# Kernel optimization log

Hardware: AMD Instinct MI355X
Metric: run time of the kernel (lower is better)

Reference implementation:

```python
import jax, jax.numpy as jnp
import numpy as np

N_NODES = 50000
N_EDGES = 600000
N_REL = 3
VALUE_NUM, TEXT_NUM, FEAT, CLASSES = 16, 768, 128, 2
N_IDX = 10000


def setup_inputs() -> dict:
    key = jax.random.key(0)
    ks = jax.random.split(key, 24)
    s = 0.05
    inp = {
        'value_feature': jax.random.normal(ks[0], (N_NODES, VALUE_NUM), jnp.float32),
        'text_feature': jax.random.normal(ks[1], (N_NODES, TEXT_NUM), jnp.float32),
        'fc1_w': jax.random.normal(ks[2], (VALUE_NUM, FEAT), jnp.float32) * s,
        'fc1_b': jnp.zeros((FEAT,), jnp.float32),
        'fc2_w': jax.random.normal(ks[3], (TEXT_NUM, FEAT), jnp.float32) * s,
        'fc2_b': jnp.zeros((FEAT,), jnp.float32),
        'relu_w': jax.random.normal(ks[4], (2 * FEAT, FEAT), jnp.float32) * s,
        'relu_b': jnp.zeros((FEAT,), jnp.float32),
        'rgcn1_wrel': jax.random.normal(ks[5], (N_REL, FEAT, FEAT), jnp.float32) * s,
        'rgcn1_wroot': jax.random.normal(ks[6], (FEAT, FEAT), jnp.float32) * s,
        'rgcn1_b': jnp.zeros((FEAT,), jnp.float32),
        'rgcn2_wrel': jax.random.normal(ks[7], (N_REL, FEAT, FEAT), jnp.float32) * s,
        'rgcn2_wroot': jax.random.normal(ks[8], (FEAT, FEAT), jnp.float32) * s,
        'rgcn2_b': jnp.zeros((FEAT,), jnp.float32),
        'fc3_w': jax.random.normal(ks[9], (FEAT, CLASSES), jnp.float32) * s,
        'fc3_b': jnp.zeros((CLASSES,), jnp.float32),
        'edge_index': jax.random.randint(ks[10], (2, N_EDGES), 0, N_NODES, jnp.int64 if jax.config.jax_enable_x64 else jnp.int32),
        'edge_type': jax.random.randint(ks[11], (N_EDGES,), 0, N_REL, jnp.int32),
        'idx': jax.random.randint(ks[12], (N_IDX,), 0, N_NODES, jnp.int32),
    }
    return inp


def _rgcn(x, w_rel, w_root, b, src, dst, etype, n_nodes):
    # Per-relation transform: [R, N, D]
    xw = jnp.einsum('nd,rde->rne', x, w_rel)
    msg = xw[etype, src]  # gather per-edge messages [E, D]
    # mean aggregation per (relation, dst) pair (PyG RGCNConv default aggr='mean')
    deg = jnp.zeros((N_REL, n_nodes), x.dtype).at[etype, dst].add(1.0)
    norm = 1.0 / jnp.maximum(deg[etype, dst], 1.0)  # [E]
    agg = jnp.zeros((n_nodes, x.shape[1]), x.dtype).at[dst].add(msg * norm[:, None])
    return agg + x @ w_root + b


def reference(value_feature, text_feature, fc1_w, fc1_b, fc2_w, fc2_b,
              relu_w, relu_b, rgcn1_wrel, rgcn1_wroot, rgcn1_b,
              rgcn2_wrel, rgcn2_wroot, rgcn2_b, fc3_w, fc3_b,
              edge_index, edge_type, idx):
    src, dst = edge_index[0], edge_index[1]
    v = value_feature @ fc1_w + fc1_b
    t = text_feature @ fc2_w + fc2_b
    h = jnp.concatenate([v, t], axis=1)
    h = jax.nn.leaky_relu(h @ relu_w + relu_b, negative_slope=0.01)
    # dropout is identity at eval
    h = _rgcn(h, rgcn1_wrel, rgcn1_wroot, rgcn1_b, src, dst, edge_type, h.shape[0])
    h = _rgcn(h, rgcn2_wrel, rgcn2_wroot, rgcn2_b, src, dst, edge_type, h.shape[0])
    return h[idx] @ fc3_w + fc3_b
```

## Files before the change

kernel.cpp:

```cpp
#include <hip/hip_runtime.h>
#include <hip/hip_bf16.h>

typedef __attribute__((ext_vector_type(8))) short s16x8;
typedef __attribute__((ext_vector_type(4))) float f32x4;
typedef unsigned short u16;
typedef unsigned int u32;

constexpr int NN = 50000;
constexpr int NE = 600000;
constexpr int NIDX = 10000;

__device__ inline u16 f2b(float x) {
    __hip_bfloat16 h = __float2bfloat16(x);
    return *(u16*)&h;
}

__device__ inline s16x8 pack8(float4 a, float4 b) {
    s16x8 r;
    r[0] = (short)f2b(a.x); r[1] = (short)f2b(a.y);
    r[2] = (short)f2b(a.z); r[3] = (short)f2b(a.w);
    r[4] = (short)f2b(b.x); r[5] = (short)f2b(b.y);
    r[6] = (short)f2b(b.z); r[7] = (short)f2b(b.w);
    return r;
}

__device__ inline void gl_lds16(const void* gptr, void* lptr) {
    __builtin_amdgcn_global_load_lds(
        (const __attribute__((address_space(1))) char*)gptr,
        (__attribute__((address_space(3))) char*)lptr, 16, 0, 0);
}

template <int N> __device__ inline void vmwait() {
    asm volatile("s_waitcnt vmcnt(%0)" :: "n"(N) : "memory");
}
__device__ inline void barrier_nodrains() {
    __builtin_amdgcn_sched_barrier(0);
    __builtin_amdgcn_s_barrier();
    __builtin_amdgcn_sched_barrier(0);
}


__global__ void k_setup(const float* __restrict__ vf,
                        const float* __restrict__ fc1w, const float* __restrict__ fc2w,
                        const float* __restrict__ reluw,
                        const float* __restrict__ fc1b, const float* __restrict__ fc2b,
                        const float* __restrict__ relub,
                        const float* __restrict__ w1rel, const float* __restrict__ w1root,
                        const float* __restrict__ w2rel, const float* __restrict__ w2root,
                        float* __restrict__ vfp, u16* __restrict__ WTin,
                        float* __restrict__ bcomb, u16* __restrict__ WT1, u16* __restrict__ WT2,
                        int* __restrict__ zero_region, int* __restrict__ mark) {
    int b = blockIdx.x, t = threadIdx.x;
    if (b < 6250) {
        int i = b * 256 + t;
        int n = i >> 5, c = i & 31;
        vfp[i] = c < 16 ? vf[n * 16 + c] : 0.f;
    } else if (b < 7050) {
        if (t < 128) {
            int k = b - 6250, c = t;
            float s = 0.f;
            if (k < 768) {
                for (int j = 0; j < 128; ++j) s += fc2w[k * 128 + j] * reluw[(128 + j) * 128 + c];
            } else if (k < 784) {
                int kk = k - 768;
                for (int j = 0; j < 128; ++j) s += fc1w[kk * 128 + j] * reluw[j * 128 + c];
            }
            WTin[c * 800 + k] = f2b(s);
        }
    } else if (b == 7050) {
        if (t < 128) {
            int c = t;
            float s = relub[c];
            for (int j = 0; j < 128; ++j) {
                s += fc1b[j] * reluw[j * 128 + c];
                s += fc2b[j] * reluw[(128 + j) * 128 + c];
            }
            bcomb[c] = s;
        }
    } else if (b < 7563) {
        if (t < 128) {
            int s = b - 7051, c = t;
            float v = (s < 384) ? w1rel[(size_t)s * 128 + c] : w1root[(size_t)(s - 384) * 128 + c];
            WT1[c * 512 + s] = f2b(v);
        }
    } else if (b < 8075) {
        if (t < 128) {
            int s = b - 7563, c = t;
            float v = (s < 384) ? w2rel[(size_t)s * 128 + c] : w2root[(size_t)(s - 384) * 128 + c];
            WT2[c * 512 + s] = f2b(v);
        }
    } else if (b < 9052) {
        int i = (b - 8075) * 256 + t;
        if (i < 250002) zero_region[i] = 0;
    } else {
        int i = (b - 9052) * 256 + t;
        if (i < NN) mark[i] = 0;
    }
}


__global__ void k_hist_mark(const int* __restrict__ ei, const int* __restrict__ et,
                            int* __restrict__ deg_node, int* __restrict__ deg_rel,
                            const int* __restrict__ idx, int* __restrict__ mark,
                            int* __restrict__ cnt2, int* __restrict__ list) {
    int b = blockIdx.x;
    if (b < 2344) {
        int e = b * 256 + threadIdx.x;
        if (e < NE) {
            int dst = ei[NE + e];
            int r = et[e];
            atomicAdd(&deg_node[dst], 1);
            atomicAdd(&deg_rel[r * NN + dst], 1);
        }
    } else {
        int i = (b - 2344) * 256 + threadIdx.x;
        if (i < NIDX) {
            int n = idx[i];
            if (atomicExch(&mark[n], 1) == 0) {
                int p = atomicAdd(cnt2, 1);
                list[p] = n;
            }
        }
    }
}


__global__ void k_alloc_norm(const int* __restrict__ deg_node, int* __restrict__ baseoff,
                             int* __restrict__ counter, const int* __restrict__ deg_rel,
                             float* __restrict__ normf) {
    int b = blockIdx.x;
    if (b < 196) {
        int i = b * 256 + threadIdx.x;
        int lane = threadIdx.x & 63;
        int d = (i < NN) ? deg_node[i] : 0;
        int scan = d;
        for (int off = 1; off < 64; off <<= 1) {
            int t = __shfl_up(scan, off, 64);
            if (lane >= off) scan += t;
        }
        int total = __shfl(scan, 63, 64);
        int wbase = 0;
        if (lane == 63) wbase = atomicAdd(counter, total);
        wbase = __shfl(wbase, 63, 64);
        if (i < NN) baseoff[i] = wbase + scan - d;
    } else {
        int i = (b - 196) * 256 + threadIdx.x;
        if (i < 3 * NN) normf[i] = 1.0f / (float)max(deg_rel[i], 1);
    }
}

__global__ void k_fill(const int* __restrict__ ei, const int* __restrict__ et,
                       const int* __restrict__ baseoff, int* __restrict__ cursor,
                       int* __restrict__ elist) {
    int e = blockIdx.x * 256 + threadIdx.x;
    if (e >= NE) return;
    int dst = ei[NE + e];
    int src = ei[e];
    int r = et[e];
    int pos = atomicAdd(&cursor[dst], 1);
    elist[baseoff[dst] + pos] = src | (r << 20);
}


__global__ __launch_bounds__(64) void k_agg(const u16* __restrict__ x, u16* __restrict__ A,
                                            const int* __restrict__ elist,
                                            const int* __restrict__ baseoff,
                                            const int* __restrict__ deg_node,
                                            const float* __restrict__ normf) {
    int n = blockIdx.x;
    int lane = threadIdx.x;
    float a0x = 0.f, a0y = 0.f, a1x = 0.f, a1y = 0.f, a2x = 0.f, a2y = 0.f;
    int nb = deg_node[n];
    int b0 = baseoff[n];
    for (int i = 0; i < nb; ++i) {
        int p = elist[b0 + i];
        int src = p & 0xFFFFF;
        int r = p >> 20;
        u32 pair = *(const u32*)&x[(size_t)src * 128 + lane * 2];
        float vx = __uint_as_float((pair & 0xFFFFu) << 16);
        float vy = __uint_as_float((pair >> 16) << 16);
        if (r == 0)      { a0x += vx; a0y += vy; }
        else if (r == 1) { a1x += vx; a1y += vy; }
        else             { a2x += vx; a2y += vy; }
    }
    float n0 = normf[n], n1 = normf[NN + n], n2 = normf[2 * NN + n];
    u32* Ao = (u32*)&A[(size_t)n * 384];
    Ao[lane]        = (u32)f2b(a0x * n0) | ((u32)f2b(a0y * n0) << 16);
    Ao[64 + lane]   = (u32)f2b(a1x * n1) | ((u32)f2b(a1y * n1) << 16);
    Ao[128 + lane]  = (u32)f2b(a2x * n2) | ((u32)f2b(a2y * n2) << 16);
}

__global__ __launch_bounds__(64) void k_agg2(const u16* __restrict__ x, u16* __restrict__ A2buf,
                                             const int* __restrict__ elist,
                                             const int* __restrict__ baseoff,
                                             const int* __restrict__ deg_node,
                                             const float* __restrict__ normf,
                                             const int* __restrict__ list,
                                             const int* __restrict__ cnt2) {
    int i = blockIdx.x;
    if (i >= *cnt2) return;
    int n = list[i];
    int lane = threadIdx.x;
    float a0x = 0.f, a0y = 0.f, a1x = 0.f, a1y = 0.f, a2x = 0.f, a2y = 0.f;
    int nb = deg_node[n];
    int b0 = baseoff[n];
    for (int e = 0; e < nb; ++e) {
        int p = elist[b0 + e];
        int src = p & 0xFFFFF;
        int r = p >> 20;
        u32 pair = *(const u32*)&x[(size_t)src * 128 + lane * 2];
        float vx = __uint_as_float((pair & 0xFFFFu) << 16);
        float vy = __uint_as_float((pair >> 16) << 16);
        if (r == 0)      { a0x += vx; a0y += vy; }
        else if (r == 1) { a1x += vx; a1y += vy; }
        else             { a2x += vx; a2y += vy; }
    }
    float n0 = normf[n], n1 = normf[NN + n], n2 = normf[2 * NN + n];
    u32* Ao = (u32*)&A2buf[(size_t)i * 384];
    Ao[lane]        = (u32)f2b(a0x * n0) | ((u32)f2b(a0y * n0) << 16);
    Ao[64 + lane]   = (u32)f2b(a1x * n1) | ((u32)f2b(a1y * n1) << 16);
    Ao[128 + lane]  = (u32)f2b(a2x * n2) | ((u32)f2b(a2y * n2) << 16);
}


template <typename TA, int K1T, int K2T, bool LRELU, bool LIST>
__device__ __forceinline__ void gemm_body(const TA* __restrict__ A1, int lda1,
                                          const TA* __restrict__ A2, int lda2,
                                          const u16* __restrict__ WT, int ldwt,
                                          const float* __restrict__ bias,
                                          u16* __restrict__ out, int Nin,
                                          const int* __restrict__ list,
                                          const int* __restrict__ cntp) {
    constexpr int KT = K1T + K2T;
    constexpr int ABYTES = 64 * 32 * (int)sizeof(TA);
    constexpr int TILEB = ABYTES + 8192;
    constexpr int OPW = (sizeof(TA) == 4) ? 4 : 3;
    __shared__ alignas(128) char lds[3][TILEB];

    const int N = LIST ? *cntp : Nin;
    const int m0 = blockIdx.x * 64;
    if (LIST && m0 >= N) return;

    const int tid = threadIdx.x;
    const int w = tid >> 6, lane = tid & 63;
    const int wr = w >> 1, wc = w & 1;
    const int lq = lane >> 4, lr = lane & 15;

    auto stage = [&](int j) {
        char* base = lds[j % 3];
        int kt = j;
        if constexpr (sizeof(TA) == 4) {
#pragma unroll
            for (int jj = 0; jj < 2; ++jj) {
                int row = w * 16 + jj * 8 + (lane >> 3);
                int s = lane & 7;
                int chunk = s ^ (row & 7);
                int rg = min(m0 + row, N - 1);
                const float* g;
                if (kt < K1T) g = (const float*)A1 + (size_t)rg * lda1 + kt * 32 + chunk * 4;
                else          g = (const float*)A2 + (size_t)rg * lda2 + (kt - K1T) * 32 + chunk * 4;
                gl_lds16(g, base + w * 2048 + jj * 1024);
            }
        } else {
            int row = w * 16 + (lane >> 2);
            int s = lane & 3;
            int chunk = s ^ ((row >> 1) & 3);
            int rg = min(m0 + row, N - 1);
            const u16* g;
            if (kt < K1T) {
                g = (const u16*)A1 + (size_t)rg * lda1 + kt * 32 + chunk * 8;
            } else {
                int node = LIST ? list[rg] : rg;
                g = (const u16*)A2 + (size_t)node * lda2 + (kt - K1T) * 32 + chunk * 8;
            }
            gl_lds16(g, base + w * 1024);
        }
#pragma unroll
        for (int jj = 0; jj < 2; ++jj) {
            int col = w * 32 + jj * 16 + (lane >> 2);
            int s = lane & 3;
            int chunk = s ^ ((col >> 1) & 3);
            const u16* g = WT + (size_t)col * ldwt + kt * 32 + chunk * 8;
            gl_lds16(g, base + ABYTES + w * 2048 + jj * 1024);
        }
    };

    f32x4 acc[2][4] = {};

    auto compute = [&](int j) {
        char* base = lds[j % 3];
        s16x8 af[2];
#pragma unroll
        for (int i = 0; i < 2; ++i) {
            int row = wr * 32 + i * 16 + lr;
            if constexpr (sizeof(TA) == 4) {
                int m = row & 7;
                float4 f0 = *(const float4*)(base + row * 128 + (((2 * lq) ^ m) * 16));
                float4 f1 = *(const float4*)(base + row * 128 + (((2 * lq + 1) ^ m) * 16));
                af[i] = pack8(f0, f1);
            } else {
                int sl = lq ^ ((row >> 1) & 3);
                af[i] = *(const s16x8*)(base + row * 64 + sl * 16);
            }
        }
#pragma unroll
        for (int j4 = 0; j4 < 4; ++j4) {
            int col = wc * 64 + j4 * 16 + lr;
            int sl = lq ^ ((col >> 1) & 3);
            s16x8 bf = *(const s16x8*)(base + ABYTES + col * 64 + sl * 16);
#pragma unroll
            for (int i = 0; i < 2; ++i)
                acc[i][j4] = __builtin_amdgcn_mfma_f32_16x16x32_bf16(af[i], bf, acc[i][j4], 0, 0, 0);
        }
    };

    stage(0); stage(1);
#pragma unroll 1
    for (int j = 0; j < KT - 1; ++j) {
        vmwait<OPW>();
        barrier_nodrains();
        if (j + 2 < KT) stage(j + 2);
        compute(j);
    }
    vmwait<0>();
    barrier_nodrains();
    compute(KT - 1);

#pragma unroll
    for (int i = 0; i < 2; ++i) {
#pragma unroll
        for (int q = 0; q < 4; ++q) {
            int grow = m0 + wr * 32 + i * 16 + lq * 4 + q;
            if (grow < N) {
                int orow = LIST ? list[grow] : grow;
#pragma unroll
                for (int j = 0; j < 4; ++j) {
                    int col = wc * 64 + j * 16 + lr;
                    float v = acc[i][j][q] + bias[col];
                    if (LRELU) v = v > 0.f ? v : 0.01f * v;
                    out[(size_t)orow * 128 + col] = f2b(v);
                }
            }
        }
    }
}

__global__ __launch_bounds__(256) void k_gemm_in(const float* __restrict__ A1, int lda1,
                                                 const float* __restrict__ A2, int lda2,
                                                 const u16* __restrict__ WT, int ldwt,
                                                 const float* __restrict__ bias,
                                                 u16* __restrict__ out, int N) {
    gemm_body<float, 24, 1, true, false>(A1, lda1, A2, lda2, WT, ldwt, bias, out, N, nullptr, nullptr);
}
__global__ __launch_bounds__(256) void k_gemm_r1(const u16* __restrict__ A1, int lda1,
                                                 const u16* __restrict__ A2, int lda2,
                                                 const u16* __restrict__ WT, int ldwt,
                                                 const float* __restrict__ bias,
                                                 u16* __restrict__ out, int N) {
    gemm_body<u16, 12, 4, false, false>(A1, lda1, A2, lda2, WT, ldwt, bias, out, N, nullptr, nullptr);
}
__global__ __launch_bounds__(256) void k_gemm_r2(const u16* __restrict__ A1, int lda1,
                                                 const u16* __restrict__ A2, int lda2,
                                                 const u16* __restrict__ WT, int ldwt,
                                                 const float* __restrict__ bias,
                                                 u16* __restrict__ out,
                                                 const int* __restrict__ list,
                                                 const int* __restrict__ cnt2) {
    gemm_body<u16, 12, 4, false, true>(A1, lda1, A2, lda2, WT, ldwt, bias, out, NIDX, list, cnt2);
}


__global__ __launch_bounds__(256) void k_out(const u16* __restrict__ h, const int* __restrict__ idx,
                                             const float* __restrict__ fc3w,
                                             const float* __restrict__ fc3b,
                                             float* __restrict__ out, int M) {
    int w = threadIdx.x >> 6;
    int lane = threadIdx.x & 63;
    int row = blockIdx.x * 4 + w;
    if (row >= M) return;
    int n = idx[row];
    u32 pair = *(const u32*)&h[(size_t)n * 128 + lane * 2];
    float v0 = __uint_as_float((pair & 0xFFFFu) << 16);
    float v1 = __uint_as_float((pair >> 16) << 16);
    float4 wv = *(const float4*)&fc3w[lane * 4];
    float s0 = v0 * wv.x + v1 * wv.z;
    float s1 = v0 * wv.y + v1 * wv.w;
    for (int off = 32; off >= 1; off >>= 1) {
        s0 += __shfl_xor(s0, off, 64);
        s1 += __shfl_xor(s1, off, 64);
    }
    if (lane == 0) {
        out[row * 2] = s0 + fc3b[0];
        out[row * 2 + 1] = s1 + fc3b[1];
    }
}


extern "C" void kernel_launch(void* const* d_in, const int* in_sizes, int n_in,
                              void* d_out, int out_size, void* d_ws, size_t ws_size,
                              hipStream_t stream) {
    const float* vf    = (const float*)d_in[0];
    const float* tf    = (const float*)d_in[1];
    const float* fc1w  = (const float*)d_in[2];
    const float* fc1b  = (const float*)d_in[3];
    const float* fc2w  = (const float*)d_in[4];
    const float* fc2b  = (const float*)d_in[5];
    const float* reluw = (const float*)d_in[6];
    const float* relub = (const float*)d_in[7];
    const float* w1rel = (const float*)d_in[8];
    const float* w1root= (const float*)d_in[9];
    const float* b1    = (const float*)d_in[10];
    const float* w2rel = (const float*)d_in[11];
    const float* w2root= (const float*)d_in[12];
    const float* b2    = (const float*)d_in[13];
    const float* fc3w  = (const float*)d_in[14];
    const float* fc3b  = (const float*)d_in[15];
    const int* ei      = (const int*)d_in[16];
    const int* et      = (const int*)d_in[17];
    const int* idx     = (const int*)d_in[18];
    float* out = (float*)d_out;

    char* W = (char*)d_ws;
    const size_t OFF_WTIN  = 0;
    const size_t OFF_WT1   = 204800;
    const size_t OFF_WT2   = 335872;
    const size_t OFF_BCOMB = 466944;
    const size_t OFF_DEGN  = 467456;
    const size_t OFF_CUR   = 667456;
    const size_t OFF_DEGR  = 867456;
    const size_t OFF_CNT   = 1467456;
    const size_t OFF_CNT2  = 1467460;
    const size_t OFF_BASE  = 1467712;
    const size_t OFF_NORM  = 1667712;
    const size_t OFF_ELIST = 2267712;
    const size_t OFF_A     = 4667712;
    const size_t OFF_H0    = 43067712;
    const size_t OFF_H1    = 55867712;
    const size_t OFF_H2    = 68667712;
    const size_t OFF_VFPAD = 81467712;
    const size_t OFF_LIST  = 87867712;
    const size_t OFF_A2    = 87907712;
    const size_t OFF_MARK  = 95587712;

    u16* WTin   = (u16*)(W + OFF_WTIN);
    u16* WT1    = (u16*)(W + OFF_WT1);
    u16* WT2    = (u16*)(W + OFF_WT2);
    float* bcomb= (float*)(W + OFF_BCOMB);
    int* degn   = (int*)(W + OFF_DEGN);
    int* cur    = (int*)(W + OFF_CUR);
    int* degr   = (int*)(W + OFF_DEGR);
    int* cnt    = (int*)(W + OFF_CNT);
    int* cnt2   = (int*)(W + OFF_CNT2);
    int* base   = (int*)(W + OFF_BASE);
    float* normf= (float*)(W + OFF_NORM);
    int* elist  = (int*)(W + OFF_ELIST);
    u16* Abuf   = (u16*)(W + OFF_A);
    u16* h0     = (u16*)(W + OFF_H0);
    u16* h1     = (u16*)(W + OFF_H1);
    u16* h2     = (u16*)(W + OFF_H2);
    float* vfp  = (float*)(W + OFF_VFPAD);
    int* list   = (int*)(W + OFF_LIST);
    u16* A2buf  = (u16*)(W + OFF_A2);
    int* mark   = (int*)(W + OFF_MARK);

    const int GRID_GEMM = (NN + 63) / 64;
    const int GRID_G2   = (NIDX + 63) / 64;

    k_setup<<<9248, 256, 0, stream>>>(vf, fc1w, fc2w, reluw, fc1b, fc2b, relub,
                                      w1rel, w1root, w2rel, w2root,
                                      vfp, WTin, bcomb, WT1, WT2, degn, mark);

    k_gemm_in<<<GRID_GEMM, 256, 0, stream>>>(tf, 768, vfp, 32, WTin, 800, bcomb, h0, NN);

    k_hist_mark<<<2384, 256, 0, stream>>>(ei, et, degn, degr, idx, mark, cnt2, list);
    k_alloc_norm<<<782, 256, 0, stream>>>(degn, base, cnt, degr, normf);
    k_fill<<<(NE + 255) / 256, 256, 0, stream>>>(ei, et, base, cur, elist);

    k_agg<<<NN, 64, 0, stream>>>(h0, Abuf, elist, base, degn, normf);
    k_gemm_r1<<<GRID_GEMM, 256, 0, stream>>>(Abuf, 384, h0, 128, WT1, 512, b1, h1, NN);

    k_agg2<<<NIDX, 64, 0, stream>>>(h1, A2buf, elist, base, degn, normf, list, cnt2);
    k_gemm_r2<<<GRID_G2, 256, 0, stream>>>(A2buf, 384, h1, 128, WT2, 512, b2, h2, list, cnt2);

    k_out<<<(NIDX + 3) / 4, 256, 0, stream>>>(h2, idx, fc3w, fc3b, out, NIDX);
}
```

Measured before the change: 246.5 us.

## Merge histogram into setup, fuse edge fill with input GEMM, memset zeroing

Zeroing of the degree, cursor, degree-by-relation, counter and mark buffers moves from kernel blocks to a single hipMemsetAsync, and the mark array is relocated so it sits in that contiguous region. The degree histogram and idx marking are folded into k_setup as extra blocks. The CSR fill then runs as extra blocks of the input GEMM kernel, which now takes an explicit block id. This cuts two kernel launches and lets the atomic-heavy fill overlap the GEMM. The risk is that the hist and mark blocks in setup share a launch with the weight prep, and fill blocks compete with GEMM blocks for compute units.

```diff
diff --git a/kernel.cpp b/kernel.cpp
--- a/kernel.cpp
+++ b/kernel.cpp
@@ -47,9 +47,12 @@
                         const float* __restrict__ relub,
                         const float* __restrict__ w1rel, const float* __restrict__ w1root,
                         const float* __restrict__ w2rel, const float* __restrict__ w2root,
+                        const int* __restrict__ ei, const int* __restrict__ et,
+                        const int* __restrict__ idx,
                         float* __restrict__ vfp, u16* __restrict__ WTin,
                         float* __restrict__ bcomb, u16* __restrict__ WT1, u16* __restrict__ WT2,
-                        int* __restrict__ zero_region, int* __restrict__ mark) {
+                        int* __restrict__ deg_node, int* __restrict__ deg_rel,
+                        int* __restrict__ mark, int* __restrict__ cnt2, int* __restrict__ list) {
     int b = blockIdx.x, t = threadIdx.x;
     if (b < 6250) {
         int i = b * 256 + t;
@@ -89,23 +92,8 @@
             float v = (s < 384) ? w2rel[(size_t)s * 128 + c] : w2root[(size_t)(s - 384) * 128 + c];
             WT2[c * 512 + s] = f2b(v);
         }
-    } else if (b < 9052) {
-        int i = (b - 8075) * 256 + t;
-        if (i < 250002) zero_region[i] = 0;
-    } else {
-        int i = (b - 9052) * 256 + t;
-        if (i < NN) mark[i] = 0;
-    }
-}
-
-
-__global__ void k_hist_mark(const int* __restrict__ ei, const int* __restrict__ et,
-                            int* __restrict__ deg_node, int* __restrict__ deg_rel,
-                            const int* __restrict__ idx, int* __restrict__ mark,
-                            int* __restrict__ cnt2, int* __restrict__ list) {
-    int b = blockIdx.x;
-    if (b < 2344) {
-        int e = b * 256 + threadIdx.x;
+    } else if (b < 10419) {
+        int e = (b - 8075) * 256 + t;
         if (e < NE) {
             int dst = ei[NE + e];
             int r = et[e];
@@ -113,7 +101,7 @@
             atomicAdd(&deg_rel[r * NN + dst], 1);
         }
     } else {
-        int i = (b - 2344) * 256 + threadIdx.x;
+        int i = (b - 10419) * 256 + t;
         if (i < NIDX) {
             int n = idx[i];
             if (atomicExch(&mark[n], 1) == 0) {
@@ -147,18 +135,6 @@
         int i = (b - 196) * 256 + threadIdx.x;
         if (i < 3 * NN) normf[i] = 1.0f / (float)max(deg_rel[i], 1);
     }
-}
-
-__global__ void k_fill(const int* __restrict__ ei, const int* __restrict__ et,
-                       const int* __restrict__ baseoff, int* __restrict__ cursor,
-                       int* __restrict__ elist) {
-    int e = blockIdx.x * 256 + threadIdx.x;
-    if (e >= NE) return;
-    int dst = ei[NE + e];
-    int src = ei[e];
-    int r = et[e];
-    int pos = atomicAdd(&cursor[dst], 1);
-    elist[baseoff[dst] + pos] = src | (r << 20);
 }
 
 
@@ -224,7 +200,8 @@
 
 
 template <typename TA, int K1T, int K2T, bool LRELU, bool LIST>
-__device__ __forceinline__ void gemm_body(const TA* __restrict__ A1, int lda1,
+__device__ __forceinline__ void gemm_body(int bid,
+                                          const TA* __restrict__ A1, int lda1,
                                           const TA* __restrict__ A2, int lda2,
                                           const u16* __restrict__ WT, int ldwt,
                                           const float* __restrict__ bias,
@@ -238,7 +215,7 @@
     __shared__ alignas(128) char lds[3][TILEB];
 
     const int N = LIST ? *cntp : Nin;
-    const int m0 = blockIdx.x * 64;
+    const int m0 = bid * 64;
     if (LIST && m0 >= N) return;
 
     const int tid = threadIdx.x;
@@ -345,19 +322,38 @@
     }
 }
 
-__global__ __launch_bounds__(256) void k_gemm_in(const float* __restrict__ A1, int lda1,
-                                                 const float* __restrict__ A2, int lda2,
-                                                 const u16* __restrict__ WT, int ldwt,
-                                                 const float* __restrict__ bias,
-                                                 u16* __restrict__ out, int N) {
-    gemm_body<float, 24, 1, true, false>(A1, lda1, A2, lda2, WT, ldwt, bias, out, N, nullptr, nullptr);
-}
+
+__global__ __launch_bounds__(256) void k_gin_fill(
+        const float* __restrict__ A1, int lda1,
+        const float* __restrict__ A2, int lda2,
+        const u16* __restrict__ WT, int ldwt,
+        const float* __restrict__ bias, u16* __restrict__ out, int N,
+        const int* __restrict__ ei, const int* __restrict__ et,
+        const int* __restrict__ baseoff, int* __restrict__ cursor,
+        int* __restrict__ elist) {
+    int b = blockIdx.x, t = threadIdx.x;
+    if (b < 782) {
+        gemm_body<float, 24, 1, true, false>(b, A1, lda1, A2, lda2, WT, ldwt,
+                                             bias, out, N, nullptr, nullptr);
+    } else {
+        int e = (b - 782) * 256 + t;
+        if (e < NE) {
+            int dst = ei[NE + e];
+            int src = ei[e];
+            int r = et[e];
+            int pos = atomicAdd(&cursor[dst], 1);
+            elist[baseoff[dst] + pos] = src | (r << 20);
+        }
+    }
+}
+
 __global__ __launch_bounds__(256) void k_gemm_r1(const u16* __restrict__ A1, int lda1,
                                                  const u16* __restrict__ A2, int lda2,
                                                  const u16* __restrict__ WT, int ldwt,
                                                  const float* __restrict__ bias,
                                                  u16* __restrict__ out, int N) {
-    gemm_body<u16, 12, 4, false, false>(A1, lda1, A2, lda2, WT, ldwt, bias, out, N, nullptr, nullptr);
+    gemm_body<u16, 12, 4, false, false>(blockIdx.x, A1, lda1, A2, lda2, WT, ldwt,
+                                        bias, out, N, nullptr, nullptr);
 }
 __global__ __launch_bounds__(256) void k_gemm_r2(const u16* __restrict__ A1, int lda1,
                                                  const u16* __restrict__ A2, int lda2,
@@ -366,7 +362,8 @@
                                                  u16* __restrict__ out,
                                                  const int* __restrict__ list,
                                                  const int* __restrict__ cnt2) {
-    gemm_body<u16, 12, 4, false, true>(A1, lda1, A2, lda2, WT, ldwt, bias, out, NIDX, list, cnt2);
+    gemm_body<u16, 12, 4, false, true>(blockIdx.x, A1, lda1, A2, lda2, WT, ldwt,
+                                       bias, out, NIDX, list, cnt2);
 }
 
 
@@ -430,17 +427,17 @@
     const size_t OFF_DEGR  = 867456;
     const size_t OFF_CNT   = 1467456;
     const size_t OFF_CNT2  = 1467460;
-    const size_t OFF_BASE  = 1467712;
-    const size_t OFF_NORM  = 1667712;
-    const size_t OFF_ELIST = 2267712;
-    const size_t OFF_A     = 4667712;
-    const size_t OFF_H0    = 43067712;
-    const size_t OFF_H1    = 55867712;
-    const size_t OFF_H2    = 68667712;
-    const size_t OFF_VFPAD = 81467712;
-    const size_t OFF_LIST  = 87867712;
-    const size_t OFF_A2    = 87907712;
-    const size_t OFF_MARK  = 95587712;
+    const size_t OFF_MARK  = 1467464;
+    const size_t OFF_BASE  = 1667520;
+    const size_t OFF_NORM  = 1867520;
+    const size_t OFF_ELIST = 2467520;
+    const size_t OFF_A     = 4867520;
+    const size_t OFF_H0    = 43267520;
+    const size_t OFF_H1    = 56067520;
+    const size_t OFF_H2    = 68867520;
+    const size_t OFF_VFPAD = 81667520;
+    const size_t OFF_LIST  = 88067520;
+    const size_t OFF_A2    = 88107520;
 
     u16* WTin   = (u16*)(W + OFF_WTIN);
     u16* WT1    = (u16*)(W + OFF_WT1);
@@ -451,6 +448,7 @@
     int* degr   = (int*)(W + OFF_DEGR);
     int* cnt    = (int*)(W + OFF_CNT);
     int* cnt2   = (int*)(W + OFF_CNT2);
+    int* mark   = (int*)(W + OFF_MARK);
     int* base   = (int*)(W + OFF_BASE);
     float* normf= (float*)(W + OFF_NORM);
     int* elist  = (int*)(W + OFF_ELIST);
@@ -461,20 +459,21 @@
     float* vfp  = (float*)(W + OFF_VFPAD);
     int* list   = (int*)(W + OFF_LIST);
     u16* A2buf  = (u16*)(W + OFF_A2);
-    int* mark   = (int*)(W + OFF_MARK);
 
     const int GRID_GEMM = (NN + 63) / 64;
     const int GRID_G2   = (NIDX + 63) / 64;
 
-    k_setup<<<9248, 256, 0, stream>>>(vf, fc1w, fc2w, reluw, fc1b, fc2b, relub,
-                                      w1rel, w1root, w2rel, w2root,
-                                      vfp, WTin, bcomb, WT1, WT2, degn, mark);
-
-    k_gemm_in<<<GRID_GEMM, 256, 0, stream>>>(tf, 768, vfp, 32, WTin, 800, bcomb, h0, NN);
-
-    k_hist_mark<<<2384, 256, 0, stream>>>(ei, et, degn, degr, idx, mark, cnt2, list);
+    hipMemsetAsync(W + OFF_DEGN, 0, 1200008, stream);
+
+    k_setup<<<10459, 256, 0, stream>>>(vf, fc1w, fc2w, reluw, fc1b, fc2b, relub,
+                                       w1rel, w1root, w2rel, w2root, ei, et, idx,
+                                       vfp, WTin, bcomb, WT1, WT2,
+                                       degn, degr, mark, cnt2, list);
+
     k_alloc_norm<<<782, 256, 0, stream>>>(degn, base, cnt, degr, normf);
-    k_fill<<<(NE + 255) / 256, 256, 0, stream>>>(ei, et, base, cur, elist);
+
+    k_gin_fill<<<3126, 256, 0, stream>>>(tf, 768, vfp, 32, WTin, 800, bcomb, h0, NN,
+                                         ei, et, base, cur, elist);
 
     k_agg<<<NN, 64, 0, stream>>>(h0, Abuf, elist, base, degn, normf);
     k_gemm_r1<<<GRID_GEMM, 256, 0, stream>>>(Abuf, 384, h0, 128, WT1, 512, b1, h1, NN);
```

Result: faster. 229.9 us (-6.7%).
